# Kernel optimization log

Measured on AMD Instinct MI355X. Metric: run time of the kernel, lower is better.

Reference implementation:

```python
import jax, jax.numpy as jnp
import numpy as np

D_MODEL = 1024
NUM_HEADS = 16
D_K = D_MODEL // NUM_HEADS


def setup_inputs() -> dict:
    key = jax.random.key(0)
    ks = jax.random.split(key, 9)
    s = 1.0 / np.sqrt(D_MODEL)
    x = jax.random.normal(ks[0], (4, 2048, D_MODEL), dtype=jnp.float32)
    Wq = jax.random.uniform(ks[1], (D_MODEL, D_MODEL), jnp.float32, -s, s)
    bq = jax.random.uniform(ks[2], (D_MODEL,), jnp.float32, -s, s)
    Wk = jax.random.uniform(ks[3], (D_MODEL, D_MODEL), jnp.float32, -s, s)
    bk = jax.random.uniform(ks[4], (D_MODEL,), jnp.float32, -s, s)
    Wv = jax.random.uniform(ks[5], (D_MODEL, D_MODEL), jnp.float32, -s, s)
    bv = jax.random.uniform(ks[6], (D_MODEL,), jnp.float32, -s, s)
    Wo = jax.random.uniform(ks[7], (D_MODEL, D_MODEL), jnp.float32, -s, s)
    bo = jax.random.uniform(ks[8], (D_MODEL,), jnp.float32, -s, s)
    return {"x": x, "Wq": Wq, "bq": bq, "Wk": Wk, "bk": bk,
            "Wv": Wv, "bv": bv, "Wo": Wo, "bo": bo}


def reference(x, Wq, bq, Wk, bk, Wv, bv, Wo, bo):
    B, S, _ = x.shape
    # project and split heads: [B,S,D] -> [B,H,S,dk]
    def heads(W, b):
        return (x @ W + b).reshape(B, S, NUM_HEADS, D_K).transpose(0, 2, 1, 3)
    q = heads(Wq, bq)
    k = heads(Wk, bk)
    v = heads(Wv, bv)
    scores = jnp.einsum('bhqd,bhkd->bhqk', q, k) / jnp.sqrt(jnp.float32(D_K))
    attn = jax.nn.softmax(scores, axis=-1)
    out = jnp.einsum('bhqk,bhkd->bhqd', attn, v)
    out = out.transpose(0, 2, 1, 3).reshape(B, S, D_MODEL)
    return out @ Wo + bo
```

## Files before the change

kernel.cpp:

```cpp
#include <hip/hip_runtime.h>
#include <hip/hip_bf16.h>

#define D_MODEL 1024
#define NUM_HEADS 16
#define D_K 64
#define B_SZ 4
#define SEQ 2048
#define SCALE_Q 0.180336881f

typedef short bf16x8 __attribute__((ext_vector_type(8)));
typedef float f32x4 __attribute__((ext_vector_type(4)));
typedef unsigned short u16;

__device__ __forceinline__ unsigned cvtpk(float a, float b) {
    unsigned r;
    asm("v_cvt_pk_bf16_f32 %0, %1, %2" : "=v"(r) : "v"(a), "v"(b));
    return r;
}
__device__ __forceinline__ u16 f2bf(float f) {
    return (u16)cvtpk(f, f);
}
__device__ __forceinline__ float exp2a(float x) {
    float r;
    asm("v_exp_f32 %0, %1" : "=v"(r) : "v"(x));
    return r;
}
__device__ __forceinline__ void gload_lds16(const u16* g, u16* l) {
    __builtin_amdgcn_global_load_lds(
        (const __attribute__((address_space(1))) unsigned int*)g,
        (__attribute__((address_space(3))) unsigned int*)l, 16, 0, 0);
}

__global__ __launch_bounds__(256) void prep_all(
    const float* __restrict__ xin, u16* __restrict__ xbf,
    const float* __restrict__ W0, const float* __restrict__ W1,
    const float* __restrict__ W2, const float* __restrict__ W3,
    u16* __restrict__ Wt)
{
    __shared__ float tile[64][65];
    const int t = threadIdx.x;
    if (blockIdx.x < 1024) {
        const int n8 = (B_SZ * SEQ * D_MODEL) / 8;
        for (int i = blockIdx.x * 256 + t; i < n8; i += 1024 * 256) {
            float4 a = ((const float4*)xin)[(size_t)i * 2];
            float4 b = ((const float4*)xin)[(size_t)i * 2 + 1];
            uint4 o;
            o.x = cvtpk(a.x, a.y);
            o.y = cvtpk(a.z, a.w);
            o.z = cvtpk(b.x, b.y);
            o.w = cvtpk(b.z, b.w);
            const int j = (i & ~3) | ((i ^ (i >> 8)) & 3);
            ((uint4*)xbf)[j] = o;
        }
        return;
    }
    const int id = blockIdx.x - 1024;
    const int z  = id >> 8;
    const int by = (id >> 4) & 15;
    const int bx = id & 15;
    const float* W = z == 0 ? W0 : z == 1 ? W1 : z == 2 ? W2 : W3;
    u16* out = Wt + (size_t)z * D_MODEL * D_MODEL;
    const int k0 = by * 64;
    const int n0 = bx * 64;
    #pragma unroll
    for (int it = 0; it < 4; ++it) {
        int idx = it * 256 + t;
        int r = idx >> 4;
        int c = (idx & 15) * 4;
        float4 v = *(const float4*)(W + (size_t)(k0 + r) * D_MODEL + n0 + c);
        tile[r][c + 0] = v.x; tile[r][c + 1] = v.y;
        tile[r][c + 2] = v.z; tile[r][c + 3] = v.w;
    }
    __syncthreads();
    #pragma unroll
    for (int it = 0; it < 2; ++it) {
        int idx = it * 256 + t;
        int r  = idx >> 3;
        int cI = idx & 7;
        int c  = cI * 8;
        uint4 o;
        o.x = cvtpk(tile[c + 0][r], tile[c + 1][r]);
        o.y = cvtpk(tile[c + 2][r], tile[c + 3][r]);
        o.z = cvtpk(tile[c + 4][r], tile[c + 5][r]);
        o.w = cvtpk(tile[c + 6][r], tile[c + 7][r]);
        const int cs = (cI & ~3) | ((cI ^ (r >> 1)) & 3);
        *(uint4*)(out + (size_t)(n0 + r) * D_MODEL + k0 + cs * 8) = o;
    }
}

__global__ __launch_bounds__(512, 4) void gemm_qkv(
    const u16* __restrict__ A, const u16* __restrict__ Wt,
    const float* __restrict__ bq, const float* __restrict__ bk,
    const float* __restrict__ bv, u16* __restrict__ Yb)
{
    __shared__ u16 As[3][128][32];
    __shared__ u16 Bs[3][128][32];
    const int t    = threadIdx.x;
    const int lane = t & 63;
    const int wid  = t >> 6;
    const int wm   = wid >> 2;
    const int wn   = wid & 3;
    const int g    = lane >> 4;
    const int lr   = lane & 15;
    const int xc   = (lr >> 1) & 3;
    const int m0   = blockIdx.y * 128;
    const int n0   = blockIdx.x * 128;
    const int K    = D_MODEL;

    const u16* Asrc = A  + (size_t)(m0 + wid * 16 + (lane >> 2)) * K + (lane & 3) * 8;
    const u16* Bsrc = Wt + (size_t)(n0 + wid * 16 + (lane >> 2)) * K + (lane & 3) * 8;

    f32x4 acc[4][2];
    #pragma unroll
    for (int i = 0; i < 4; ++i)
        #pragma unroll
        for (int j = 0; j < 2; ++j)
            acc[i][j] = (f32x4){0.f, 0.f, 0.f, 0.f};

    gload_lds16(Asrc,      &As[0][wid * 16][0]);
    gload_lds16(Bsrc,      &Bs[0][wid * 16][0]);
    gload_lds16(Asrc + 32, &As[1][wid * 16][0]);
    gload_lds16(Bsrc + 32, &Bs[1][wid * 16][0]);

    #pragma unroll
    for (int k = 0; k < 32; ++k) {
        if (k < 31) asm volatile("s_waitcnt vmcnt(2)" ::: "memory");
        else        asm volatile("s_waitcnt vmcnt(0)" ::: "memory");
        __builtin_amdgcn_s_barrier();
        __builtin_amdgcn_sched_barrier(0);
        if (k + 2 < 32) {
            const int nb = (k + 2) % 3;
            gload_lds16(Asrc + (k + 2) * 32, &As[nb][wid * 16][0]);
            gload_lds16(Bsrc + (k + 2) * 32, &Bs[nb][wid * 16][0]);
        }
        const int cb = k % 3;
        bf16x8 af[4], bfr[2];
        #pragma unroll
        for (int mt = 0; mt < 4; ++mt)
            af[mt] = *(const bf16x8*)(&As[cb][wm * 64 + mt * 16 + lr][(g ^ xc) * 8]);
        #pragma unroll
        for (int nt = 0; nt < 2; ++nt)
            bfr[nt] = *(const bf16x8*)(&Bs[cb][wn * 32 + nt * 16 + lr][(g ^ xc) * 8]);
        #pragma unroll
        for (int mt = 0; mt < 4; ++mt)
            #pragma unroll
            for (int nt = 0; nt < 2; ++nt)
                acc[mt][nt] = __builtin_amdgcn_mfma_f32_16x16x32_bf16(
                    af[mt], bfr[nt], acc[mt][nt], 0, 0, 0);
    }

    const int which = n0 >> 10;
    const float scale = (which == 0) ? SCALE_Q : 1.0f;
    const float* bp = (which == 0) ? bq : (which == 1) ? bk : bv;
    u16* dst = Yb + (size_t)which * ((size_t)B_SZ * SEQ * D_MODEL);

    float bv2[2];
    #pragma unroll
    for (int nt = 0; nt < 2; ++nt)
        bv2[nt] = bp[((n0 + wn * 32 + nt * 16 + lr) & 1023)];

    #pragma unroll
    for (int mt = 0; mt < 4; ++mt) {
        #pragma unroll
        for (int nt = 0; nt < 2; ++nt) {
            float v4[4];
            #pragma unroll
            for (int r = 0; r < 4; ++r) v4[r] = (acc[mt][nt][r] + bv2[nt]) * scale;
            const int mbase = m0 + wm * 64 + mt * 16 + g * 4;
            const int nn = (n0 + wn * 32 + nt * 16 + lr) & 1023;
            const int h = nn >> 6, d = nn & 63;
            const int bb = mbase >> 11, s2 = mbase & 2047;
            if (which == 2) {
                const int z  = s2 & 63;
                const int zp = (z & 32) + 8 * ((z & 15) >> 2) + 4 * ((z >> 4) & 1);
                const int col = zp ^ ((d & 7) << 3);
                uint2 o;
                o.x = cvtpk(v4[0], v4[1]);
                o.y = cvtpk(v4[2], v4[3]);
                *(uint2*)&dst[(((size_t)(bb * NUM_HEADS + h) * D_K + d) * SEQ) + (s2 & ~63) + col] = o;
            } else {
                #pragma unroll
                for (int r = 0; r < 4; ++r) {
                    const int s2r = s2 + r;
                    const int dd = (which == 1) ? (d ^ ((s2r & 7) << 3)) : d;
                    dst[(((size_t)(bb * NUM_HEADS + h) * SEQ) + s2r) * D_K + dd] = f2bf(v4[r]);
                }
            }
        }
    }
}

__global__ __launch_bounds__(512, 4) void gemm_o(
    const u16* __restrict__ A, const u16* __restrict__ Wt,
    const float* __restrict__ bias, float* __restrict__ Y)
{
    __shared__ u16 As[3][128][32];
    __shared__ u16 Bs[3][128][32];
    const int t    = threadIdx.x;
    const int lane = t & 63;
    const int wid  = t >> 6;
    const int wm   = wid >> 2;
    const int wn   = wid & 3;
    const int g    = lane >> 4;
    const int lr   = lane & 15;
    const int xc   = (lr >> 1) & 3;
    const int m0   = blockIdx.y * 128;
    const int n0   = blockIdx.x * 128;
    const int K    = D_MODEL;

    const u16* Asrc = A  + (size_t)(m0 + wid * 16 + (lane >> 2)) * K + (lane & 3) * 8;
    const u16* Bsrc = Wt + (size_t)(n0 + wid * 16 + (lane >> 2)) * K + (lane & 3) * 8;

    f32x4 acc[4][2];
    #pragma unroll
    for (int i = 0; i < 4; ++i)
        #pragma unroll
        for (int j = 0; j < 2; ++j)
            acc[i][j] = (f32x4){0.f, 0.f, 0.f, 0.f};

    gload_lds16(Asrc,      &As[0][wid * 16][0]);
    gload_lds16(Bsrc,      &Bs[0][wid * 16][0]);
    gload_lds16(Asrc + 32, &As[1][wid * 16][0]);
    gload_lds16(Bsrc + 32, &Bs[1][wid * 16][0]);

    #pragma unroll
    for (int k = 0; k < 32; ++k) {
        if (k < 31) asm volatile("s_waitcnt vmcnt(2)" ::: "memory");
        else        asm volatile("s_waitcnt vmcnt(0)" ::: "memory");
        __builtin_amdgcn_s_barrier();
        __builtin_amdgcn_sched_barrier(0);
        if (k + 2 < 32) {
            const int nb = (k + 2) % 3;
            gload_lds16(Asrc + (k + 2) * 32, &As[nb][wid * 16][0]);
            gload_lds16(Bsrc + (k + 2) * 32, &Bs[nb][wid * 16][0]);
        }
        const int cb = k % 3;
        bf16x8 af[4], bfr[2];
        #pragma unroll
        for (int mt = 0; mt < 4; ++mt)
            af[mt] = *(const bf16x8*)(&As[cb][wm * 64 + mt * 16 + lr][(g ^ xc) * 8]);
        #pragma unroll
        for (int nt = 0; nt < 2; ++nt)
            bfr[nt] = *(const bf16x8*)(&Bs[cb][wn * 32 + nt * 16 + lr][(g ^ xc) * 8]);
        #pragma unroll
        for (int mt = 0; mt < 4; ++mt)
            #pragma unroll
            for (int nt = 0; nt < 2; ++nt)
                acc[mt][nt] = __builtin_amdgcn_mfma_f32_16x16x32_bf16(
                    af[mt], bfr[nt], acc[mt][nt], 0, 0, 0);
    }

    float bv2[2];
    #pragma unroll
    for (int nt = 0; nt < 2; ++nt) bv2[nt] = bias[n0 + wn * 32 + nt * 16 + lr];

    #pragma unroll
    for (int mt = 0; mt < 4; ++mt)
        #pragma unroll
        for (int nt = 0; nt < 2; ++nt)
            #pragma unroll
            for (int r = 0; r < 4; ++r) {
                const int m = m0 + wm * 64 + mt * 16 + g * 4 + r;
                const int n = n0 + wn * 32 + nt * 16 + lr;
                Y[(size_t)m * D_MODEL + n] = acc[mt][nt][r] + bv2[nt];
            }
}

__global__ __launch_bounds__(512, 4) void attn_mfma(
    const u16* __restrict__ Q, const u16* __restrict__ Kb,
    const u16* __restrict__ Vt, u16* __restrict__ ctx)
{
    __shared__ u16 Ks[2][128][64];
    __shared__ u16 Vs[2][64][128];
    const int t    = threadIdx.x;
    const int lane = t & 63;
    const int w    = t >> 6;
    const int g    = lane >> 4;
    const int lr   = lane & 15;
    const int fid  = blockIdx.x + (blockIdx.y << 3) + (blockIdx.z << 7);
    const int oid  = (fid & 7) * 64 + (fid >> 3);
    const int qt   = oid & 7;
    const int h    = (oid >> 3) & 15;
    const int b    = oid >> 7;
    const size_t hoff = ((size_t)b * NUM_HEADS + h) * SEQ * D_K;

    bf16x8 qf[2][2];
    #pragma unroll
    for (int u = 0; u < 2; ++u) {
        const int q = qt * 256 + w * 32 + u * 16 + lr;
        qf[u][0] = *(const bf16x8*)(Q + hoff + (size_t)q * D_K + g * 8);
        qf[u][1] = *(const bf16x8*)(Q + hoff + (size_t)q * D_K + g * 8 + 32);
    }

    bf16x8 onesf;
    #pragma unroll
    for (int j = 0; j < 8; ++j) onesf[j] = (short)0x3F80;

    const int krow = w * 16 + (lane >> 3);
    const int kcol = (lane & 7) * 8;
    const u16* ksrc = Kb + hoff + (size_t)krow * D_K + kcol;
    const int vrow = w * 8 + (lane >> 4);
    const int vcol = (lane & 15) * 8;
    const u16* vsrc = Vt + hoff + (size_t)vrow * SEQ + vcol;

    const int xm = (lr & 7) << 3;

    f32x4 acc_o[2][4];
    f32x4 acc_l[2];
    #pragma unroll
    for (int u = 0; u < 2; ++u) {
        acc_l[u] = (f32x4){0.f, 0.f, 0.f, 0.f};
        #pragma unroll
        for (int n = 0; n < 4; ++n) acc_o[u][n] = (f32x4){0.f, 0.f, 0.f, 0.f};
    }

    gload_lds16(ksrc,               &Ks[0][w * 16][0]);
    gload_lds16(ksrc + 8 * D_K,     &Ks[0][w * 16 + 8][0]);
    gload_lds16(vsrc,               &Vs[0][w * 8][0]);
    gload_lds16(vsrc + 4 * SEQ,     &Vs[0][w * 8 + 4][0]);

    int bu = 0;
    for (int kt = 0; kt < SEQ / 128; ++kt) {
        __syncthreads();
        if (kt + 1 < SEQ / 128) {
            const size_t kv0 = (size_t)(kt + 1) * 128;
            const int nb = bu ^ 1;
            gload_lds16(ksrc + kv0 * D_K,       &Ks[nb][w * 16][0]);
            gload_lds16(ksrc + (kv0 + 8) * D_K, &Ks[nb][w * 16 + 8][0]);
            gload_lds16(vsrc + kv0,             &Vs[nb][w * 8][0]);
            gload_lds16(vsrc + 4 * SEQ + kv0,   &Vs[nb][w * 8 + 4][0]);
        }

        #pragma unroll
        for (int hv = 0; hv < 2; ++hv) {
            f32x4 sc[2][4];
            #pragma unroll
            for (int u = 0; u < 2; ++u)
                #pragma unroll
                for (int mt = 0; mt < 4; ++mt) sc[u][mt] = (f32x4){0.f, 0.f, 0.f, 0.f};
            __builtin_amdgcn_s_setprio(1);
            #pragma unroll
            for (int s = 0; s < 2; ++s)
                #pragma unroll
                for (int mt = 0; mt < 4; ++mt) {
                    bf16x8 kf = *(const bf16x8*)(
                        &Ks[bu][hv * 64 + mt * 16 + lr][(g * 8 + s * 32) ^ xm]);
                    sc[0][mt] = __builtin_amdgcn_mfma_f32_16x16x32_bf16(kf, qf[0][s], sc[0][mt], 0, 0, 0);
                    sc[1][mt] = __builtin_amdgcn_mfma_f32_16x16x32_bf16(kf, qf[1][s], sc[1][mt], 0, 0, 0);
                }
            __builtin_amdgcn_s_setprio(0);

            union { bf16x8 v; unsigned u[4]; } pa[2][2];
            #pragma unroll
            for (int u = 0; u < 2; ++u) {
                #pragma unroll
                for (int mt = 0; mt < 4; ++mt)
                    #pragma unroll
                    for (int r = 0; r < 4; ++r)
                        sc[u][mt][r] = exp2a(sc[u][mt][r]);
                #pragma unroll
                for (int s = 0; s < 2; ++s) {
                    pa[u][s].u[0] = cvtpk(sc[u][2 * s][0],     sc[u][2 * s][1]);
                    pa[u][s].u[1] = cvtpk(sc[u][2 * s][2],     sc[u][2 * s][3]);
                    pa[u][s].u[2] = cvtpk(sc[u][2 * s + 1][0], sc[u][2 * s + 1][1]);
                    pa[u][s].u[3] = cvtpk(sc[u][2 * s + 1][2], sc[u][2 * s + 1][3]);
                }
            }

            __builtin_amdgcn_s_setprio(1);
            #pragma unroll
            for (int s = 0; s < 2; ++s) {
                #pragma unroll
                for (int n = 0; n < 4; ++n) {
                    bf16x8 vf = *(const bf16x8*)(
                        &Vs[bu][16 * n + lr][hv * 64 + ((32 * s + 8 * g) ^ xm)]);
                    acc_o[0][n] = __builtin_amdgcn_mfma_f32_16x16x32_bf16(pa[0][s].v, vf, acc_o[0][n], 0, 0, 0);
                    acc_o[1][n] = __builtin_amdgcn_mfma_f32_16x16x32_bf16(pa[1][s].v, vf, acc_o[1][n], 0, 0, 0);
                }
                acc_l[0] = __builtin_amdgcn_mfma_f32_16x16x32_bf16(pa[0][s].v, onesf, acc_l[0], 0, 0, 0);
                acc_l[1] = __builtin_amdgcn_mfma_f32_16x16x32_bf16(pa[1][s].v, onesf, acc_l[1], 0, 0, 0);
            }
            __builtin_amdgcn_s_setprio(0);
        }
        bu ^= 1;
    }

    #pragma unroll
    for (int u = 0; u < 2; ++u) {
        f32x4 linv;
        #pragma unroll
        for (int r = 0; r < 4; ++r) linv[r] = 1.0f / acc_l[u][r];
        #pragma unroll
        for (int n = 0; n < 4; ++n)
            #pragma unroll
            for (int r = 0; r < 4; ++r) {
                const int qrow = qt * 256 + w * 32 + u * 16 + 4 * g + r;
                const int cbase = h * D_K + 16 * n + lr;
                const int ch  = cbase >> 3;
                const int ch2 = (ch & ~3) | ((ch ^ (qrow >> 1)) & 3);
                ctx[((size_t)b * SEQ + qrow) * D_MODEL + (ch2 << 3) + (cbase & 7)] =
                    f2bf(acc_o[u][n][r] * linv[r]);
            }
    }
}

extern "C" void kernel_launch(void* const* d_in, const int* in_sizes, int n_in,
                              void* d_out, int out_size, void* d_ws, size_t ws_size,
                              hipStream_t stream)
{
    const float* x  = (const float*)d_in[0];
    const float* Wq = (const float*)d_in[1];
    const float* bq = (const float*)d_in[2];
    const float* Wk = (const float*)d_in[3];
    const float* bk = (const float*)d_in[4];
    const float* Wv = (const float*)d_in[5];
    const float* bv = (const float*)d_in[6];
    const float* Wo = (const float*)d_in[7];
    const float* bo = (const float*)d_in[8];
    float* out = (float*)d_out;

    char* ws = (char*)d_ws;
    const size_t MB = 1024 * 1024;
    u16* xbf  = (u16*)(ws);
    u16* Wt   = (u16*)(ws + 16 * MB);
    u16* Qbf  = (u16*)(ws + 24 * MB);
    u16* ctxb = (u16*)(ws + 72 * MB);
    u16* Kbf  = Qbf + (size_t)B_SZ * SEQ * D_MODEL;
    u16* Vtw  = Kbf + (size_t)B_SZ * SEQ * D_MODEL;

    prep_all<<<2048, 256, 0, stream>>>(x, xbf, Wq, Wk, Wv, Wo, Wt);

    gemm_qkv<<<dim3(3 * D_MODEL / 128, (B_SZ * SEQ) / 128), 512, 0, stream>>>(
        xbf, Wt, bq, bk, bv, Qbf);

    attn_mfma<<<dim3(SEQ / 256, NUM_HEADS, B_SZ), 512, 0, stream>>>(Qbf, Kbf, Vtw, ctxb);

    gemm_o<<<dim3(D_MODEL / 128, (B_SZ * SEQ) / 128), 512, 0, stream>>>(
        ctxb, Wt + 3 * (size_t)D_MODEL * D_MODEL, bo, out);
}
```

Before: 169.1 us.

## Widen output-projection GEMM K-tile to 64 with double buffering and new swizzle

The output-projection GEMM moves from a triple-buffered 32-wide K tile to a double-buffered 64-wide K tile, using a row-based XOR swizzle that covers all 8 chunks. The Wo transpose and the attention context writes are changed to store in the matching pre-swizzled layout. The aim is half as many barrier-separated iterations and more MFMA work per sync. In exchange the shared memory use is larger, the occupancy hint is dropped, and it relies on plain __syncthreads instead of fine-grained vmcnt pipelining.

Result: no change. 167.2 us (-1.1%).

```diff
diff --git a/kernel.cpp b/kernel.cpp
--- a/kernel.cpp
+++ b/kernel.cpp
@@ -83,7 +83,9 @@
         o.y = cvtpk(tile[c + 2][r], tile[c + 3][r]);
         o.z = cvtpk(tile[c + 4][r], tile[c + 5][r]);
         o.w = cvtpk(tile[c + 6][r], tile[c + 7][r]);
-        const int cs = (cI & ~3) | ((cI ^ (r >> 1)) & 3);
+        int cs;
+        if (z == 3) cs = cI ^ (r & 7);
+        else        cs = (cI & ~3) | ((cI ^ (r >> 1)) & 3);
         *(uint4*)(out + (size_t)(n0 + r) * D_MODEL + k0 + cs * 8) = o;
     }
 }
@@ -190,12 +192,12 @@
     }
 }
 
-__global__ __launch_bounds__(512, 4) void gemm_o(
+__global__ __launch_bounds__(512) void gemm_o(
     const u16* __restrict__ A, const u16* __restrict__ Wt,
     const float* __restrict__ bias, float* __restrict__ Y)
 {
-    __shared__ u16 As[3][128][32];
-    __shared__ u16 Bs[3][128][32];
+    __shared__ u16 As[2][128][64];
+    __shared__ u16 Bs[2][128][64];
     const int t    = threadIdx.x;
     const int lane = t & 63;
     const int wid  = t >> 6;
@@ -203,13 +205,13 @@
     const int wn   = wid & 3;
     const int g    = lane >> 4;
     const int lr   = lane & 15;
-    const int xc   = (lr >> 1) & 3;
     const int m0   = blockIdx.y * 128;
     const int n0   = blockIdx.x * 128;
     const int K    = D_MODEL;
-
-    const u16* Asrc = A  + (size_t)(m0 + wid * 16 + (lane >> 2)) * K + (lane & 3) * 8;
-    const u16* Bsrc = Wt + (size_t)(n0 + wid * 16 + (lane >> 2)) * K + (lane & 3) * 8;
+    const int xm   = (lr & 7) << 3;
+
+    const int srow8 = lane >> 3;
+    const int scol  = (lane & 7) * 8;
 
     f32x4 acc[4][2];
     #pragma unroll
@@ -218,36 +220,42 @@
         for (int j = 0; j < 2; ++j)
             acc[i][j] = (f32x4){0.f, 0.f, 0.f, 0.f};
 
-    gload_lds16(Asrc,      &As[0][wid * 16][0]);
-    gload_lds16(Bsrc,      &Bs[0][wid * 16][0]);
-    gload_lds16(Asrc + 32, &As[1][wid * 16][0]);
-    gload_lds16(Bsrc + 32, &Bs[1][wid * 16][0]);
-
-    #pragma unroll
-    for (int k = 0; k < 32; ++k) {
-        if (k < 31) asm volatile("s_waitcnt vmcnt(2)" ::: "memory");
-        else        asm volatile("s_waitcnt vmcnt(0)" ::: "memory");
-        __builtin_amdgcn_s_barrier();
-        __builtin_amdgcn_sched_barrier(0);
-        if (k + 2 < 32) {
-            const int nb = (k + 2) % 3;
-            gload_lds16(Asrc + (k + 2) * 32, &As[nb][wid * 16][0]);
-            gload_lds16(Bsrc + (k + 2) * 32, &Bs[nb][wid * 16][0]);
-        }
-        const int cb = k % 3;
-        bf16x8 af[4], bfr[2];
-        #pragma unroll
-        for (int mt = 0; mt < 4; ++mt)
-            af[mt] = *(const bf16x8*)(&As[cb][wm * 64 + mt * 16 + lr][(g ^ xc) * 8]);
-        #pragma unroll
-        for (int nt = 0; nt < 2; ++nt)
-            bfr[nt] = *(const bf16x8*)(&Bs[cb][wn * 32 + nt * 16 + lr][(g ^ xc) * 8]);
-        #pragma unroll
-        for (int mt = 0; mt < 4; ++mt)
+    #pragma unroll
+    for (int it = 0; it < 2; ++it) {
+        const int seg = it * 8 + wid;
+        gload_lds16(A  + (size_t)(m0 + seg * 8 + srow8) * K + scol, &As[0][seg * 8][0]);
+        gload_lds16(Wt + (size_t)(n0 + seg * 8 + srow8) * K + scol, &Bs[0][seg * 8][0]);
+    }
+    __syncthreads();
+
+    for (int k0 = 0; k0 < K; k0 += 64) {
+        const int cur = (k0 >> 6) & 1;
+        if (k0 + 64 < K) {
+            const int nb = cur ^ 1;
+            #pragma unroll
+            for (int it = 0; it < 2; ++it) {
+                const int seg = it * 8 + wid;
+                gload_lds16(A  + (size_t)(m0 + seg * 8 + srow8) * K + k0 + 64 + scol, &As[nb][seg * 8][0]);
+                gload_lds16(Wt + (size_t)(n0 + seg * 8 + srow8) * K + k0 + 64 + scol, &Bs[nb][seg * 8][0]);
+            }
+        }
+        #pragma unroll
+        for (int s = 0; s < 2; ++s) {
+            bf16x8 af[4], bfr[2];
+            #pragma unroll
+            for (int mt = 0; mt < 4; ++mt)
+                af[mt] = *(const bf16x8*)(&As[cur][wm * 64 + mt * 16 + lr][(g * 8 + s * 32) ^ xm]);
             #pragma unroll
             for (int nt = 0; nt < 2; ++nt)
-                acc[mt][nt] = __builtin_amdgcn_mfma_f32_16x16x32_bf16(
-                    af[mt], bfr[nt], acc[mt][nt], 0, 0, 0);
+                bfr[nt] = *(const bf16x8*)(&Bs[cur][wn * 32 + nt * 16 + lr][(g * 8 + s * 32) ^ xm]);
+            #pragma unroll
+            for (int mt = 0; mt < 4; ++mt)
+                #pragma unroll
+                for (int nt = 0; nt < 2; ++nt)
+                    acc[mt][nt] = __builtin_amdgcn_mfma_f32_16x16x32_bf16(
+                        af[mt], bfr[nt], acc[mt][nt], 0, 0, 0);
+        }
+        __syncthreads();
     }
 
     float bv2[2];
@@ -395,10 +403,8 @@
             #pragma unroll
             for (int r = 0; r < 4; ++r) {
                 const int qrow = qt * 256 + w * 32 + u * 16 + 4 * g + r;
-                const int cbase = h * D_K + 16 * n + lr;
-                const int ch  = cbase >> 3;
-                const int ch2 = (ch & ~3) | ((ch ^ (qrow >> 1)) & 3);
-                ctx[((size_t)b * SEQ + qrow) * D_MODEL + (ch2 << 3) + (cbase & 7)] =
+                const int col  = (h * D_K + 16 * n + lr) ^ ((qrow & 7) << 3);
+                ctx[((size_t)b * SEQ + qrow) * D_MODEL + col] =
                     f2bf(acc_o[u][n][r] * linv[r]);
             }
     }
```
